# Performance work log

Hardware: AMD Instinct MI355X
Metric: run time of the kernel (lower is better)

## Reference

```python
import jax, jax.numpy as jnp
import numpy as np

EPS = float(np.finfo(np.float32).eps)
BN_EPS = 1e-5
TOP_K = 3


def _dist_squared(p1, p2):
    # p1: [B,N,3], p2: [B,S,3] -> [B,N,S]
    d = -2.0 * jnp.einsum('bnc,bsc->bns', p1, p2)
    d = d + jnp.sum(p1 * p1, axis=-1, keepdims=True)
    d = d + jnp.sum(p2 * p2, axis=-1)[:, None, :]
    return d


def _bn_gelu(x, gamma, beta):
    # training-mode BatchNorm1d over (batch, points), then exact GELU
    m = jnp.mean(x, axis=(0, 1))
    v = jnp.var(x, axis=(0, 1))
    xn = (x - m) * jax.lax.rsqrt(v + BN_EPS)
    return jax.nn.gelu(xn * gamma + beta, approximate=False)


def setup_inputs() -> dict:
    key = jax.random.key(0)
    ks = jax.random.split(key, 8)
    B, S, N, F, C = 8, 2048, 8192, 256, 128
    d_in, d_h, d_out = C + F, 512, 512
    return {
        'super_xyz': jax.random.normal(ks[0], (B, S, 3), jnp.float32),
        'super_point_features': jax.random.normal(ks[1], (B, S, F), jnp.float32),
        'xyz': jax.random.normal(ks[2], (B, N, 3), jnp.float32),
        'point_features': jax.random.normal(ks[3], (B, N, C), jnp.float32),
        'W1': jax.random.normal(ks[4], (d_in, d_h), jnp.float32) * 0.02,
        'g1': jnp.ones((d_h,), jnp.float32),
        'b1': jnp.zeros((d_h,), jnp.float32),
        'W2': jax.random.normal(ks[5], (d_h, d_out), jnp.float32) * 0.02,
        'g2': jnp.ones((d_out,), jnp.float32),
        'b2': jnp.zeros((d_out,), jnp.float32),
    }


def reference(super_xyz, super_point_features, xyz, point_features,
              W1, g1, b1, W2, g2, b2):
    d2 = _dist_squared(xyz, super_xyz)                 # [B,N,S]
    neg_vals, idx = jax.lax.top_k(-d2, TOP_K)          # smallest-k
    dists = jnp.maximum(-neg_vals, 0.0)                # [B,N,K]
    w = 1.0 / (dists + EPS)
    w = w / jnp.sum(w, axis=2, keepdims=True)
    gathered = jax.vmap(lambda f, i: f[i])(super_point_features, idx)  # [B,N,K,F]
    interp = jnp.sum(gathered * w[..., None], axis=2)  # [B,N,F]
    x = jnp.concatenate([point_features, interp], axis=-1)
    x = _bn_gelu(x @ W1, g1, b1)
    x = _bn_gelu(x @ W2, g2, b2)
    return x
```

## Files before the change

### kernel.cpp

```cpp
#include <hip/hip_runtime.h>
#include <hip/hip_bf16.h>


#define MROWS 65536
#define SPTS  2048
#define NPTS  8192
#define NCHUNK 8
#define CHUNK  (SPTS / NCHUNK)
#define EPSF  1.1920928955078125e-07f

typedef __bf16 v8bf __attribute__((ext_vector_type(8)));
typedef float  v4f  __attribute__((ext_vector_type(4)));

__device__ __forceinline__ float bf2f(unsigned short u) {
    union { unsigned u; float f; } v; v.u = ((unsigned)u) << 16; return v.f;
}
__device__ __forceinline__ unsigned short f2bf(float f) {
    union { float f; unsigned u; } v; v.f = f;
    unsigned r = v.u + 0x7fffu + ((v.u >> 16) & 1u);
    return (unsigned short)(r >> 16);
}
__device__ __forceinline__ float2 bf2x(unsigned u) {
    union { unsigned q; float f; } lo, hi;
    lo.q = u << 16; hi.q = u & 0xffff0000u;
    return make_float2(lo.f, hi.f);
}
__device__ __forceinline__ float ldf(const void* p, size_t i, bool bf) {
    return bf ? bf2f(((const unsigned short*)p)[i]) : ((const float*)p)[i];
}
__device__ __forceinline__ bool is_bf16_flag(const unsigned* dt) {
    return *dt == 0x3F803F80u;
}
__device__ __forceinline__ void gld16(const unsigned short* g, unsigned short* l) {
    __builtin_amdgcn_global_load_lds((const __attribute__((address_space(1))) void*)g,
                                     (__attribute__((address_space(3))) void*)l, 16, 0, 0);
}
__device__ __forceinline__ unsigned wmix(unsigned a, unsigned b, unsigned c,
                                         float w0, float w1, float w2) {
    float2 fa = bf2x(a), fb = bf2x(b), fc = bf2x(c);
    float lo = w0 * fa.x + w1 * fb.x + w2 * fc.x;
    float hi = w0 * fa.y + w1 * fb.y + w2 * fc.y;
    return ((unsigned)f2bf(hi) << 16) | (unsigned)f2bf(lo);
}
__device__ __forceinline__ uint2 pack4(float4 v) {
    uint2 r;
    r.x = ((unsigned)f2bf(v.y) << 16) | (unsigned)f2bf(v.x);
    r.y = ((unsigned)f2bf(v.w) << 16) | (unsigned)f2bf(v.z);
    return r;
}

__global__ __launch_bounds__(256) void transpose_w(const void* __restrict__ W,
                                                   unsigned short* __restrict__ WT,
                                                   int K, int N, const unsigned* dt) {
    bool bf = is_bf16_flag(dt);
    int idx = blockIdx.x * 256 + threadIdx.x;
    if (idx >= K * N) return;
    int n = idx / K, k = idx - n * K;
    WT[idx] = f2bf(ldf(W, (size_t)k * N + n, bf));
}

__global__ __launch_bounds__(256) void knn_scan(const void* __restrict__ sxyz_g,
                                                const void* __restrict__ xyz_g,
                                                double* __restrict__ pd,
                                                int* __restrict__ pi,
                                                const unsigned* dt) {
    const bool bf = is_bf16_flag(dt);
    __shared__ double4 sc[CHUNK];
    const int b = blockIdx.y, c = blockIdx.z, tid = threadIdx.x;

    {
        int s = c * CHUNK + tid;
        size_t off = ((size_t)b * SPTS + s) * 3;
        float x, y, z;
        if (bf) {
            const unsigned short* p = (const unsigned short*)sxyz_g + off;
            x = bf2f(p[0]); y = bf2f(p[1]); z = bf2f(p[2]);
        } else {
            const float* p = (const float*)sxyz_g + off;
            x = p[0]; y = p[1]; z = p[2];
        }
        double dx = (double)x, dy = (double)y, dz = (double)z;
        double4 v;
        v.x = -2.0 * dx; v.y = -2.0 * dy; v.z = -2.0 * dz;
        v.w = dx * dx + dy * dy + dz * dz;
        sc[tid] = v;
    }
    __syncthreads();

    const int nA = blockIdx.x * 512 + tid;
    const int nB = nA + 256;
    double ax, ay, az, bx, by, bz;
    {
        size_t offA = ((size_t)b * NPTS + nA) * 3;
        size_t offB = ((size_t)b * NPTS + nB) * 3;
        if (bf) {
            const unsigned short* pA = (const unsigned short*)xyz_g + offA;
            const unsigned short* pB = (const unsigned short*)xyz_g + offB;
            ax = (double)bf2f(pA[0]); ay = (double)bf2f(pA[1]); az = (double)bf2f(pA[2]);
            bx = (double)bf2f(pB[0]); by = (double)bf2f(pB[1]); bz = (double)bf2f(pB[2]);
        } else {
            const float* pA = (const float*)xyz_g + offA;
            const float* pB = (const float*)xyz_g + offB;
            ax = (double)pA[0]; ay = (double)pA[1]; az = (double)pA[2];
            bx = (double)pB[0]; by = (double)pB[1]; bz = (double)pB[2];
        }
    }
    const double na = ax * ax + ay * ay + az * az;
    const double nb = bx * bx + by * by + bz * bz;

    double a0 = 1e300, a1 = 1e300, a2 = 1e300;
    double q0 = 1e300, q1 = 1e300, q2 = 1e300;
    int ai0 = 0, ai1 = 0, ai2 = 0, bi0 = 0, bi1 = 0, bi2 = 0;
    #pragma unroll 4
    for (int s = 0; s < CHUNK; ++s) {
        double4 v = sc[s];
        double da = fma(ax, v.x, fma(ay, v.y, fma(az, v.z, v.w)));
        double db = fma(bx, v.x, fma(by, v.y, fma(bz, v.z, v.w)));
        if (da < a2) {
            int gi = c * CHUNK + s;
            if (da < a1) {
                a2 = a1; ai2 = ai1;
                if (da < a0) { a1 = a0; ai1 = ai0; a0 = da; ai0 = gi; }
                else         { a1 = da; ai1 = gi; }
            } else { a2 = da; ai2 = gi; }
        }
        if (db < q2) {
            int gi = c * CHUNK + s;
            if (db < q1) {
                q2 = q1; bi2 = bi1;
                if (db < q0) { q1 = q0; bi1 = bi0; q0 = db; bi0 = gi; }
                else         { q1 = db; bi1 = gi; }
            } else { q2 = db; bi2 = gi; }
        }
    }
    size_t baseA = ((size_t)c * MROWS + (size_t)b * NPTS + nA) * 3;
    size_t baseB = ((size_t)c * MROWS + (size_t)b * NPTS + nB) * 3;
    pd[baseA] = a0 + na; pd[baseA + 1] = a1 + na; pd[baseA + 2] = a2 + na;
    pi[baseA] = ai0; pi[baseA + 1] = ai1; pi[baseA + 2] = ai2;
    pd[baseB] = q0 + nb; pd[baseB + 1] = q1 + nb; pd[baseB + 2] = q2 + nb;
    pi[baseB] = bi0; pi[baseB + 1] = bi1; pi[baseB + 2] = bi2;
}

__global__ __launch_bounds__(256) void knn_weights(const double* __restrict__ pd,
                                                   const int* __restrict__ pi,
                                                   char* __restrict__ wi) {
    const int g = blockIdx.x * 256 + threadIdx.x;

    double d0 = 1e300, d1 = 1e300, d2 = 1e300;
    int i0 = 0, i1 = 0, i2 = 0;
    #pragma unroll
    for (int c = 0; c < NCHUNK; ++c) {
        size_t base = ((size_t)c * MROWS + g) * 3;
        #pragma unroll
        for (int j = 0; j < 3; ++j) {
            double d = pd[base + j];
            int gi = pi[base + j];
            if (d < d2) {
                if (d < d1) {
                    d2 = d1; i2 = i1;
                    if (d < d0) { d1 = d0; i1 = i0; d0 = d; i0 = gi; }
                    else        { d1 = d;  i1 = gi; }
                } else { d2 = d; i2 = gi; }
            }
        }
    }
    d0 = d0 > 0.0 ? d0 : 0.0;
    d1 = d1 > 0.0 ? d1 : 0.0;
    d2 = d2 > 0.0 ? d2 : 0.0;
    const double ED = (double)EPSF;
    double w0d = 1.0 / (d0 + ED), w1d = 1.0 / (d1 + ED), w2d = 1.0 / (d2 + ED);
    double wsd = w0d + w1d + w2d;
    float w0 = (float)(w0d / wsd), w1 = (float)(w1d / wsd), w2 = (float)(w2d / wsd);

    uint4 iv; iv.x = (unsigned)i0; iv.y = (unsigned)i1; iv.z = (unsigned)i2; iv.w = 0u;
    float4 wv = make_float4(w0, w1, w2, 0.0f);
    *(uint4*)(wi + (size_t)g * 32) = iv;
    *(float4*)(wi + (size_t)g * 32 + 16) = wv;
}

__global__ __launch_bounds__(256) void knn_interp(const char* __restrict__ wi,
                                                  const void* __restrict__ spf_g,
                                                  const void* __restrict__ pf_g,
                                                  unsigned short* __restrict__ x0,
                                                  const unsigned* dt) {
    const bool bf = is_bf16_flag(dt);
    const int tid = threadIdx.x;
    const int pl  = tid >> 4;
    const int sub = tid & 15;
    const int g   = blockIdx.x * 16 + pl;
    const int b   = g >> 13;

    const uint4  iv = *(const uint4*)(wi + (size_t)g * 32);
    const float4 wv = *(const float4*)(wi + (size_t)g * 32 + 16);
    const int i0 = (int)iv.x, i1 = (int)iv.y, i2 = (int)iv.z;
    const float w0 = wv.x, w1 = wv.y, w2 = wv.z;

    unsigned short* xr = x0 + (size_t)g * 384;
    uint4* xo = (uint4*)xr;

    if (bf) {
        const uint4* pp = (const uint4*)((const unsigned short*)pf_g + (size_t)g * 128);
        xo[sub] = pp[sub];
        const unsigned short* sb = (const unsigned short*)spf_g + (size_t)b * SPTS * 256;
        const uint4* fa = (const uint4*)(sb + (size_t)i0 * 256);
        const uint4* fb = (const uint4*)(sb + (size_t)i1 * 256);
        const uint4* fc = (const uint4*)(sb + (size_t)i2 * 256);
        #pragma unroll
        for (int r = 0; r < 2; ++r) {
            int j = sub + 16 * r;
            uint4 ua = fa[j], ub = fb[j], uc = fc[j], o;
            o.x = wmix(ua.x, ub.x, uc.x, w0, w1, w2);
            o.y = wmix(ua.y, ub.y, uc.y, w0, w1, w2);
            o.z = wmix(ua.z, ub.z, uc.z, w0, w1, w2);
            o.w = wmix(ua.w, ub.w, uc.w, w0, w1, w2);
            xo[16 + j] = o;
        }
    } else {
        const float4* pp = (const float4*)((const float*)pf_g + (size_t)g * 128);
        float4 v0 = pp[2 * sub], v1 = pp[2 * sub + 1];
        uint2 pa = pack4(v0), pb = pack4(v1);
        uint4 w; w.x = pa.x; w.y = pa.y; w.z = pb.x; w.w = pb.y;
        xo[sub] = w;
        const float* sb = (const float*)spf_g + (size_t)b * SPTS * 256;
        const float4* fa = (const float4*)(sb + (size_t)i0 * 256);
        const float4* fb = (const float4*)(sb + (size_t)i1 * 256);
        const float4* fc = (const float4*)(sb + (size_t)i2 * 256);
        #pragma unroll
        for (int r = 0; r < 2; ++r) {
            int j = sub + 16 * r;
            float4 a0 = fa[2 * j], a1 = fa[2 * j + 1];
            float4 b0 = fb[2 * j], b1 = fb[2 * j + 1];
            float4 c0 = fc[2 * j], c1 = fc[2 * j + 1];
            float4 r0, r1;
            r0.x = w0 * a0.x + w1 * b0.x + w2 * c0.x;
            r0.y = w0 * a0.y + w1 * b0.y + w2 * c0.y;
            r0.z = w0 * a0.z + w1 * b0.z + w2 * c0.z;
            r0.w = w0 * a0.w + w1 * b0.w + w2 * c0.w;
            r1.x = w0 * a1.x + w1 * b1.x + w2 * c1.x;
            r1.y = w0 * a1.y + w1 * b1.y + w2 * c1.y;
            r1.z = w0 * a1.z + w1 * b1.z + w2 * c1.z;
            r1.w = w0 * a1.w + w1 * b1.w + w2 * c1.w;
            uint2 p0 = pack4(r0), p1 = pack4(r1);
            uint4 o; o.x = p0.x; o.y = p0.y; o.z = p1.x; o.w = p1.y;
            xo[16 + j] = o;
        }
    }
}

template<bool CF32>
__global__ __launch_bounds__(256) void gemm_bt(const unsigned short* __restrict__ A,
                                               const unsigned short* __restrict__ BT,
                                               void* __restrict__ C,
                                               int M, int N, int K,
                                               float* __restrict__ gsum,
                                               float* __restrict__ gsq) {
    __shared__ unsigned short As[128 * 32];
    __shared__ unsigned short Bs[128 * 32];
    const int tid = threadIdx.x;
    const int m0 = blockIdx.x * 128, n0 = blockIdx.y * 128;
    const int lane = tid & 63, wave = tid >> 6;
    const int wm = (wave >> 1) * 64, wn = (wave & 1) * 64;
    const int l15 = lane & 15, quad = lane >> 4;

    const int o0 = tid * 16, o1 = o0 + 4096;
    const int ar0 = o0 >> 6, ac0 = (o0 & 63) >> 1;
    const int ar1 = o1 >> 6, ac1 = (o1 & 63) >> 1;
    const unsigned short* a0 = A + (size_t)(m0 + ar0) * K + ac0;
    const unsigned short* a1 = A + (size_t)(m0 + ar1) * K + ac1;
    const unsigned short* b0 = BT + (size_t)(n0 + ar0) * K + ac0;
    const unsigned short* b1 = BT + (size_t)(n0 + ar1) * K + ac1;
    unsigned short* la0 = &As[o0 >> 1];
    unsigned short* la1 = &As[o1 >> 1];
    unsigned short* lb0 = &Bs[o0 >> 1];
    unsigned short* lb1 = &Bs[o1 >> 1];

    v4f acc[4][4] = {};
    for (int k0 = 0; k0 < K; k0 += 32) {
        gld16(a0 + k0, la0);
        gld16(a1 + k0, la1);
        gld16(b0 + k0, lb0);
        gld16(b1 + k0, lb1);
        __syncthreads();
        v8bf af[4], bfr[4];
        #pragma unroll
        for (int t = 0; t < 4; ++t)
            af[t] = *(const v8bf*)&As[(wm + t * 16 + l15) * 32 + quad * 8];
        #pragma unroll
        for (int u = 0; u < 4; ++u)
            bfr[u] = *(const v8bf*)&Bs[(wn + u * 16 + l15) * 32 + quad * 8];
        #pragma unroll
        for (int t = 0; t < 4; ++t)
            #pragma unroll
            for (int u = 0; u < 4; ++u)
                acc[t][u] = __builtin_amdgcn_mfma_f32_16x16x32_bf16(af[t], bfr[u], acc[t][u], 0, 0, 0);
        __syncthreads();
    }
    #pragma unroll
    for (int t = 0; t < 4; ++t) {
        int row = m0 + wm + t * 16 + quad * 4;
        #pragma unroll
        for (int u = 0; u < 4; ++u) {
            int col = n0 + wn + u * 16 + l15;
            #pragma unroll
            for (int r = 0; r < 4; ++r) {
                if (CF32) ((float*)C)[(size_t)(row + r) * N + col] = acc[t][u][r];
                else ((unsigned short*)C)[(size_t)(row + r) * N + col] = f2bf(acc[t][u][r]);
            }
        }
    }

    float s4[4], q4[4];
    #pragma unroll
    for (int u = 0; u < 4; ++u) {
        float s = 0.0f, q = 0.0f;
        #pragma unroll
        for (int t = 0; t < 4; ++t)
            #pragma unroll
            for (int r = 0; r < 4; ++r) {
                float v = acc[t][u][r];
                s += v; q += v * v;
            }
        s4[u] = s; q4[u] = q;
    }
    #pragma unroll
    for (int u = 0; u < 4; ++u) {
        s4[u] += __shfl_xor(s4[u], 16);
        s4[u] += __shfl_xor(s4[u], 32);
        q4[u] += __shfl_xor(q4[u], 16);
        q4[u] += __shfl_xor(q4[u], 32);
    }
    float* cs = (float*)As;
    float* cq = (float*)Bs;
    __syncthreads();
    if (quad == 0) {
        #pragma unroll
        for (int u = 0; u < 4; ++u) {
            cs[wave * 64 + u * 16 + l15] = s4[u];
            cq[wave * 64 + u * 16 + l15] = q4[u];
        }
    }
    __syncthreads();
    if (tid < 128) {
        int hf = tid >> 6, idx = tid & 63;
        float ss = cs[hf * 64 + idx] + cs[(hf + 2) * 64 + idx];
        float qq = cq[hf * 64 + idx] + cq[(hf + 2) * 64 + idx];
        atomicAdd(&gsum[n0 + tid], ss);
        atomicAdd(&gsq[n0 + tid], qq);
    }
}

__global__ __launch_bounds__(256) void bn_finalize(float* __restrict__ gsum, float* __restrict__ gsq,
                                                   float* __restrict__ scale, float* __restrict__ shift,
                                                   const void* __restrict__ g, const void* __restrict__ bta,
                                                   const unsigned* dt, float invM) {
    bool bf = is_bf16_flag(dt);
    int c = blockIdx.x * 256 + threadIdx.x;
    float mean = gsum[c] * invM;
    float var  = gsq[c] * invM - mean * mean;
    float rstd = rsqrtf(var + 1e-5f);
    float gv = ldf(g, c, bf), bv = ldf(bta, c, bf);
    scale[c] = gv * rstd;
    shift[c] = bv - mean * gv * rstd;
    gsum[c] = 0.0f; gsq[c] = 0.0f;
}

template<bool F32IN>
__global__ __launch_bounds__(256) void bn_gelu(const void* __restrict__ yv,
                                               const float* __restrict__ scale,
                                               const float* __restrict__ shift,
                                               void* __restrict__ outp,
                                               const unsigned* dt) {
    bool outf32 = false;
    if (dt) outf32 = !is_bf16_flag(dt);
    size_t gid = (size_t)blockIdx.x * 256 + threadIdx.x;
    size_t base = gid * 8;
    int c0 = (int)(base & 511);
    float in[8];
    if (F32IN) {
        const float4* yp = (const float4*)((const float*)yv + base);
        float4 v0 = yp[0], v1 = yp[1];
        in[0] = v0.x; in[1] = v0.y; in[2] = v0.z; in[3] = v0.w;
        in[4] = v1.x; in[5] = v1.y; in[6] = v1.z; in[7] = v1.w;
    } else {
        uint4 v = *(const uint4*)((const unsigned short*)yv + base);
        float2 f0 = bf2x(v.x), f1 = bf2x(v.y), f2 = bf2x(v.z), f3 = bf2x(v.w);
        in[0] = f0.x; in[1] = f0.y; in[2] = f1.x; in[3] = f1.y;
        in[4] = f2.x; in[5] = f2.y; in[6] = f3.x; in[7] = f3.y;
    }
    float4 sc0 = *(const float4*)&scale[c0];
    float4 sc1 = *(const float4*)&scale[c0 + 4];
    float4 sh0 = *(const float4*)&shift[c0];
    float4 sh1 = *(const float4*)&shift[c0 + 4];
    float sc[8] = {sc0.x, sc0.y, sc0.z, sc0.w, sc1.x, sc1.y, sc1.z, sc1.w};
    float sh[8] = {sh0.x, sh0.y, sh0.z, sh0.w, sh1.x, sh1.y, sh1.z, sh1.w};
    float o[8];
    #pragma unroll
    for (int j = 0; j < 8; ++j) {
        float x = in[j] * sc[j] + sh[j];
        o[j] = 0.5f * x * (1.0f + erff(x * 0.70710678118654752f));
    }
    if (!outf32) {
        uint4 w;
        w.x = ((unsigned)f2bf(o[1]) << 16) | (unsigned)f2bf(o[0]);
        w.y = ((unsigned)f2bf(o[3]) << 16) | (unsigned)f2bf(o[2]);
        w.z = ((unsigned)f2bf(o[5]) << 16) | (unsigned)f2bf(o[4]);
        w.w = ((unsigned)f2bf(o[7]) << 16) | (unsigned)f2bf(o[6]);
        *(uint4*)((unsigned short*)outp + base) = w;
    } else {
        float4 w0 = make_float4(o[0], o[1], o[2], o[3]);
        float4 w1 = make_float4(o[4], o[5], o[6], o[7]);
        ((float4*)outp)[gid * 2] = w0;
        ((float4*)outp)[gid * 2 + 1] = w1;
    }
}

extern "C" void kernel_launch(void* const* d_in, const int* in_sizes, int n_in,
                              void* d_out, int out_size, void* d_ws, size_t ws_size,
                              hipStream_t stream) {
    const void* sxyz = d_in[0];
    const void* spf  = d_in[1];
    const void* xyz  = d_in[2];
    const void* pf   = d_in[3];
    const void* W1   = d_in[4];
    const unsigned* dt = (const unsigned*)d_in[5];
    const void* b1   = d_in[6];
    const void* W2   = d_in[7];
    const void* g2   = d_in[8];
    const void* b2   = d_in[9];

    char* ws = (char*)d_ws;
    const size_t X0_BYTES = 50331648;
    const size_t YF_BYTES = 134217728;
    const size_t PD_BYTES = (size_t)MROWS * NCHUNK * 3 * 8;
    const size_t PI_BYTES = (size_t)MROWS * NCHUNK * 3 * 4;
    const size_t NEED_F32 = X0_BYTES + YF_BYTES + 393216 + 524288 + 8192;

    if (ws_size >= NEED_F32) {
        unsigned short* x0  = (unsigned short*)ws;
        float* yF           = (float*)(ws + X0_BYTES);
        double* pd          = (double*)(ws + X0_BYTES);
        int* pi             = (int*)(ws + X0_BYTES + PD_BYTES);
        char* wi            = (char*)(ws + X0_BYTES + PD_BYTES + PI_BYTES);
        unsigned short* w1t = (unsigned short*)(ws + X0_BYTES + YF_BYTES);
        unsigned short* w2t = (unsigned short*)(ws + X0_BYTES + YF_BYTES + 393216);
        float* stats        = (float*)(ws + X0_BYTES + YF_BYTES + 393216 + 524288);
        float* gsum = stats, *gsq = stats + 512, *scale = stats + 1024, *shift = stats + 1536;
        unsigned short* x1 = (unsigned short*)d_out;

        hipMemsetAsync(gsum, 0, 4096, stream);
        transpose_w<<<dim3((384 * 512 + 255) / 256), 256, 0, stream>>>(W1, w1t, 384, 512, dt);
        transpose_w<<<dim3((512 * 512 + 255) / 256), 256, 0, stream>>>(W2, w2t, 512, 512, dt);
        knn_scan<<<dim3(16, 8, NCHUNK), 256, 0, stream>>>(sxyz, xyz, pd, pi, dt);
        knn_weights<<<dim3(256), 256, 0, stream>>>(pd, pi, wi);
        knn_interp<<<dim3(4096), 256, 0, stream>>>(wi, spf, pf, x0, dt);
        gemm_bt<true><<<dim3(512, 4), 256, 0, stream>>>(x0, w1t, yF, MROWS, 512, 384, gsum, gsq);
        bn_finalize<<<2, 256, 0, stream>>>(gsum, gsq, scale, shift, d_in[5], b1, dt, 1.0f / 65536.0f);
        bn_gelu<true><<<16384, 256, 0, stream>>>(yF, scale, shift, x1, nullptr);
        gemm_bt<true><<<dim3(512, 4), 256, 0, stream>>>(x1, w2t, yF, MROWS, 512, 512, gsum, gsq);
        bn_finalize<<<2, 256, 0, stream>>>(gsum, gsq, scale, shift, g2, b2, dt, 1.0f / 65536.0f);
        bn_gelu<true><<<16384, 256, 0, stream>>>(yF, scale, shift, d_out, dt);
    } else {
        unsigned short* x0  = (unsigned short*)ws;
        unsigned short* y2  = (unsigned short*)ws;
        char* wi            = (char*)(ws + X0_BYTES);
        unsigned short* w1t = (unsigned short*)(ws + 67108864);
        unsigned short* w2t = (unsigned short*)(ws + 67108864 + 393216);
        float* stats = (float*)(ws + 67108864 + 393216 + 524288);
        float* gsum = stats, *gsq = stats + 512, *scale = stats + 1024, *shift = stats + 1536;
        double* pd = (double*)(ws + 67108864 + 393216 + 524288 + 8192);
        int* pi    = (int*)(ws + 67108864 + 393216 + 524288 + 8192 + PD_BYTES);
        unsigned short* y1 = (unsigned short*)d_out;

        hipMemsetAsync(gsum, 0, 4096, stream);
        transpose_w<<<dim3((384 * 512 + 255) / 256), 256, 0, stream>>>(W1, w1t, 384, 512, dt);
        transpose_w<<<dim3((512 * 512 + 255) / 256), 256, 0, stream>>>(W2, w2t, 512, 512, dt);
        knn_scan<<<dim3(16, 8, NCHUNK), 256, 0, stream>>>(sxyz, xyz, pd, pi, dt);
        knn_weights<<<dim3(256), 256, 0, stream>>>(pd, pi, wi);
        knn_interp<<<dim3(4096), 256, 0, stream>>>(wi, spf, pf, x0, dt);
        gemm_bt<false><<<dim3(512, 4), 256, 0, stream>>>(x0, w1t, y1, MROWS, 512, 384, gsum, gsq);
        bn_finalize<<<2, 256, 0, stream>>>(gsum, gsq, scale, shift, d_in[5], b1, dt, 1.0f / 65536.0f);
        bn_gelu<false><<<16384, 256, 0, stream>>>(y1, scale, shift, y1, nullptr);
        gemm_bt<false><<<dim3(512, 4), 256, 0, stream>>>(y1, w2t, y2, MROWS, 512, 512, gsum, gsq);
        bn_finalize<<<2, 256, 0, stream>>>(gsum, gsq, scale, shift, g2, b2, dt, 1.0f / 65536.0f);
        bn_gelu<false><<<16384, 256, 0, stream>>>(y2, scale, shift, d_out, dt);
    }
}
```

Baseline: 515.6 us.

## Double-buffer GEMM LDS tiles and swap grid order for A-tile reuse

Measured after the change: 486.9 us. 1.06x faster.

```diff
diff --git a/kernel.cpp b/kernel.cpp
--- a/kernel.cpp
+++ b/kernel.cpp
@@ -254,47 +254,57 @@
                                                int M, int N, int K,
                                                float* __restrict__ gsum,
                                                float* __restrict__ gsq) {
-    __shared__ unsigned short As[128 * 32];
-    __shared__ unsigned short Bs[128 * 32];
+    __shared__ unsigned short As[2][4096];
+    __shared__ unsigned short Bs[2][4096];
     const int tid = threadIdx.x;
-    const int m0 = blockIdx.x * 128, n0 = blockIdx.y * 128;
+    const int n0 = blockIdx.x * 128, m0 = blockIdx.y * 128;
     const int lane = tid & 63, wave = tid >> 6;
     const int wm = (wave >> 1) * 64, wn = (wave & 1) * 64;
     const int l15 = lane & 15, quad = lane >> 4;
 
     const int o0 = tid * 16, o1 = o0 + 4096;
+    const int s0 = o0 >> 1, s1 = o1 >> 1;
     const int ar0 = o0 >> 6, ac0 = (o0 & 63) >> 1;
     const int ar1 = o1 >> 6, ac1 = (o1 & 63) >> 1;
     const unsigned short* a0 = A + (size_t)(m0 + ar0) * K + ac0;
     const unsigned short* a1 = A + (size_t)(m0 + ar1) * K + ac1;
     const unsigned short* b0 = BT + (size_t)(n0 + ar0) * K + ac0;
     const unsigned short* b1 = BT + (size_t)(n0 + ar1) * K + ac1;
-    unsigned short* la0 = &As[o0 >> 1];
-    unsigned short* la1 = &As[o1 >> 1];
-    unsigned short* lb0 = &Bs[o0 >> 1];
-    unsigned short* lb1 = &Bs[o1 >> 1];
-
+
+    const int nt = K >> 5;
     v4f acc[4][4] = {};
-    for (int k0 = 0; k0 < K; k0 += 32) {
-        gld16(a0 + k0, la0);
-        gld16(a1 + k0, la1);
-        gld16(b0 + k0, lb0);
-        gld16(b1 + k0, lb1);
-        __syncthreads();
+
+    gld16(a0, &As[0][s0]);
+    gld16(a1, &As[0][s1]);
+    gld16(b0, &Bs[0][s0]);
+    gld16(b1, &Bs[0][s1]);
+    __syncthreads();
+
+    int cur = 0;
+    for (int t = 0; t < nt; ++t) {
+        if (t + 1 < nt) {
+            int k0 = (t + 1) << 5;
+            gld16(a0 + k0, &As[cur ^ 1][s0]);
+            gld16(a1 + k0, &As[cur ^ 1][s1]);
+            gld16(b0 + k0, &Bs[cur ^ 1][s0]);
+            gld16(b1 + k0, &Bs[cur ^ 1][s1]);
+        }
         v8bf af[4], bfr[4];
         #pragma unroll
-        for (int t = 0; t < 4; ++t)
-            af[t] = *(const v8bf*)&As[(wm + t * 16 + l15) * 32 + quad * 8];
+        for (int t2 = 0; t2 < 4; ++t2)
+            af[t2] = *(const v8bf*)&As[cur][(wm + t2 * 16 + l15) * 32 + quad * 8];
         #pragma unroll
         for (int u = 0; u < 4; ++u)
-            bfr[u] = *(const v8bf*)&Bs[(wn + u * 16 + l15) * 32 + quad * 8];
-        #pragma unroll
-        for (int t = 0; t < 4; ++t)
+            bfr[u] = *(const v8bf*)&Bs[cur][(wn + u * 16 + l15) * 32 + quad * 8];
+        #pragma unroll
+        for (int t2 = 0; t2 < 4; ++t2)
             #pragma unroll
             for (int u = 0; u < 4; ++u)
-                acc[t][u] = __builtin_amdgcn_mfma_f32_16x16x32_bf16(af[t], bfr[u], acc[t][u], 0, 0, 0);
+                acc[t2][u] = __builtin_amdgcn_mfma_f32_16x16x32_bf16(af[t2], bfr[u], acc[t2][u], 0, 0, 0);
         __syncthreads();
-    }
+        cur ^= 1;
+    }
+
     #pragma unroll
     for (int t = 0; t < 4; ++t) {
         int row = m0 + wm + t * 16 + quad * 4;
@@ -329,8 +339,8 @@
         q4[u] += __shfl_xor(q4[u], 16);
         q4[u] += __shfl_xor(q4[u], 32);
     }
-    float* cs = (float*)As;
-    float* cq = (float*)Bs;
+    float* cs = (float*)&As[0][0];
+    float* cq = (float*)&Bs[0][0];
     __syncthreads();
     if (quad == 0) {
         #pragma unroll
@@ -453,10 +463,10 @@
         knn_scan<<<dim3(16, 8, NCHUNK), 256, 0, stream>>>(sxyz, xyz, pd, pi, dt);
         knn_weights<<<dim3(256), 256, 0, stream>>>(pd, pi, wi);
         knn_interp<<<dim3(4096), 256, 0, stream>>>(wi, spf, pf, x0, dt);
-        gemm_bt<true><<<dim3(512, 4), 256, 0, stream>>>(x0, w1t, yF, MROWS, 512, 384, gsum, gsq);
+        gemm_bt<true><<<dim3(4, 512), 256, 0, stream>>>(x0, w1t, yF, MROWS, 512, 384, gsum, gsq);
         bn_finalize<<<2, 256, 0, stream>>>(gsum, gsq, scale, shift, d_in[5], b1, dt, 1.0f / 65536.0f);
         bn_gelu<true><<<16384, 256, 0, stream>>>(yF, scale, shift, x1, nullptr);
-        gemm_bt<true><<<dim3(512, 4), 256, 0, stream>>>(x1, w2t, yF, MROWS, 512, 512, gsum, gsq);
+        gemm_bt<true><<<dim3(4, 512), 256, 0, stream>>>(x1, w2t, yF, MROWS, 512, 512, gsum, gsq);
         bn_finalize<<<2, 256, 0, stream>>>(gsum, gsq, scale, shift, g2, b2, dt, 1.0f / 65536.0f);
         bn_gelu<true><<<16384, 256, 0, stream>>>(yF, scale, shift, d_out, dt);
     } else {
@@ -477,10 +487,10 @@
         knn_scan<<<dim3(16, 8, NCHUNK), 256, 0, stream>>>(sxyz, xyz, pd, pi, dt);
         knn_weights<<<dim3(256), 256, 0, stream>>>(pd, pi, wi);
         knn_interp<<<dim3(4096), 256, 0, stream>>>(wi, spf, pf, x0, dt);
-        gemm_bt<false><<<dim3(512, 4), 256, 0, stream>>>(x0, w1t, y1, MROWS, 512, 384, gsum, gsq);
+        gemm_bt<false><<<dim3(4, 512), 256, 0, stream>>>(x0, w1t, y1, MROWS, 512, 384, gsum, gsq);
         bn_finalize<<<2, 256, 0, stream>>>(gsum, gsq, scale, shift, d_in[5], b1, dt, 1.0f / 65536.0f);
         bn_gelu<false><<<16384, 256, 0, stream>>>(y1, scale, shift, y1, nullptr);
-        gemm_bt<false><<<dim3(512, 4), 256, 0, stream>>>(y1, w2t, y2, MROWS, 512, 512, gsum, gsq);
+        gemm_bt<false><<<dim3(4, 512), 256, 0, stream>>>(y1, w2t, y2, MROWS, 512, 512, gsum, gsq);
         bn_finalize<<<2, 256, 0, stream>>>(gsum, gsq, scale, shift, g2, b2, dt, 1.0f / 65536.0f);
         bn_gelu<false><<<16384, 256, 0, stream>>>(y2, scale, shift, d_out, dt);
     }
```
